# Optimization experiments

Hardware: AMD Instinct MI355X
Metric: run time of the kernel (lower is better)

Reference implementation:

```python
import jax, jax.numpy as jnp
import numpy as np


def setup_inputs() -> dict:
    key = jax.random.key(0)
    kx, kw = jax.random.split(key)
    batch, n_in, n_out = 8192, 4096, 4096
    x = jax.random.normal(kx, (batch, n_in), dtype=jnp.float32)
    stdv = 1.0 / np.sqrt(n_in)
    w = jax.random.normal(kw, (n_in, n_out), dtype=jnp.float32) * stdv
    return {"x": x, "w": w}


def reference(x, w):
    # fp16_grad forward: fp32 -> fp16 -> fp32 round trip on weights
    w16 = w.astype(jnp.float16).astype(jnp.float32)
    # binarize_weight forward: sign(clip(w, -1, 1))  (STE only affects backward)
    wb = jnp.sign(jnp.clip(w16, -1.0, 1.0))
    # dense matmul with binarized weights: [B, n_in] @ [n_in, n_out]
    return x @ wb
```

## Files before the change

### kernel.cpp

```cpp
#include <hip/hip_runtime.h>
#include <hip/hip_fp16.h>

#define MM 8192
#define NN 4096
#define KK 4096
#define BM 256
#define BN 256
#define BK 64
#define NT (KK / BK)

typedef __attribute__((ext_vector_type(8))) short bf16x8;
typedef __attribute__((ext_vector_type(4))) float floatx4;
typedef __attribute__((ext_vector_type(8))) unsigned short ushort8_t;

typedef const __attribute__((address_space(1))) unsigned int* gptr_t;
typedef __attribute__((address_space(3))) unsigned int* lptr_t;

__device__ __forceinline__ unsigned short f2bf(float f) {
    unsigned u = __builtin_bit_cast(unsigned, f);
    u += 0x7FFFu + ((u >> 16) & 1u);
    return (unsigned short)(u >> 16);
}

__device__ __forceinline__ unsigned short sign_bf16(float f) {
    float h = __half2float(__float2half(f));
    return (h > 0.f) ? 0x3F80u : ((h < 0.f) ? 0xBF80u : 0u);
}

__global__ __launch_bounds__(256) void cvt_x_kernel(const float4* __restrict__ x4,
                                                    ushort4* __restrict__ o4, int n4) {
    int i = blockIdx.x * 256 + threadIdx.x;
    if (i >= n4) return;
    float4 v = x4[i];
    ushort4 o;
    o.x = f2bf(v.x); o.y = f2bf(v.y); o.z = f2bf(v.z); o.w = f2bf(v.w);
    o4[i] = o;
}

__global__ __launch_bounds__(256) void binz_wt_kernel(const float* __restrict__ w,
                                                      unsigned short* __restrict__ wt) {
    __shared__ unsigned short tileT[64][72];
    const int n0 = blockIdx.x * 64;
    const int k0 = blockIdx.y * 64;
    const int t  = threadIdx.x;
    {
        const int c4 = t & 15;
        const int rb = t >> 4;
#pragma unroll
        for (int i = 0; i < 4; ++i) {
            int r = rb + i * 16;
            float4 v = *(const float4*)&w[(size_t)(k0 + r) * NN + n0 + c4 * 4];
            tileT[c4 * 4 + 0][r] = sign_bf16(v.x);
            tileT[c4 * 4 + 1][r] = sign_bf16(v.y);
            tileT[c4 * 4 + 2][r] = sign_bf16(v.z);
            tileT[c4 * 4 + 3][r] = sign_bf16(v.w);
        }
    }
    __syncthreads();
    {
        const int g  = t & 7;
        const int nb = t >> 3;
#pragma unroll
        for (int i = 0; i < 2; ++i) {
            int n = nb + i * 32;
            *(ushort8_t*)&wt[(size_t)(n0 + n) * KK + k0 + g * 8] =
                *(const ushort8_t*)&tileT[n][g * 8];
        }
    }
}

__global__ __launch_bounds__(512, 2) void gemm_bin_kernel(const unsigned short* __restrict__ A,
                                                          const unsigned short* __restrict__ Bt,
                                                          float* __restrict__ C) {
    __shared__ __align__(16) char lds[131072];

    const int tid    = threadIdx.x;
    const int lane   = tid & 63;
    const int wave   = tid >> 6;
    const int wave_u = __builtin_amdgcn_readfirstlane(wave);
    const int wm     = wave >> 2;
    const int wn     = wave & 3;
    const int l15    = lane & 15;
    const int kq     = lane >> 4;

    const int bid = blockIdx.x;
    const int wg  = (bid & 7) * 64 + (bid >> 3);
    const int bn0 = (wg & 15) * BN;
    const int bm0 = (wg >> 4) * BM;

    const int r0 = tid >> 3;
    const int c0 = (tid & 7) ^ (r0 & 7);
    const char* gA = (const char*)A;
    const char* gB = (const char*)Bt;
    const size_t aoff = (size_t)(bm0 + r0) * (KK * 2) + (size_t)c0 * 16;
    const size_t boff = (size_t)(bn0 + r0) * (KK * 2) + (size_t)c0 * 16;

    __attribute__((address_space(3))) char* lds3 =
        (__attribute__((address_space(3))) char*)lds;
    const int dstw = wave_u * 1024;

    const int aco0 = ((0 * 4 + kq) ^ (lane & 7)) * 16;
    const int aco1 = ((1 * 4 + kq) ^ (lane & 7)) * 16;
    const char* ldsA_l = lds + l15 * 128;
    const char* ldsB_l = lds + 65536 + ((wn & 1) * 64 + l15) * 128;

    floatx4 acc[8][4] = {};
    bf16x8 af[8][2];
    bf16x8 bfr[4][2];

    auto STAGE_A = [&](int h, int kt) {
        const int slot = (kt & 1) * 2 + h;
        const char* s0 = gA + aoff + (size_t)h * (128 * KK * 2) + (size_t)kt * (BK * 2);
        __builtin_amdgcn_global_load_lds((gptr_t)s0,
            (lptr_t)(lds3 + slot * 16384 + dstw), 16, 0, 0);
        __builtin_amdgcn_global_load_lds((gptr_t)(s0 + (size_t)64 * KK * 2),
            (lptr_t)(lds3 + slot * 16384 + 8192 + dstw), 16, 0, 0);
    };
    auto STAGE_B = [&](int h, int kt) {
        const int slot = (kt & 1) * 2 + h;
        const char* s0 = gB + boff + (size_t)h * (128 * KK * 2) + (size_t)kt * (BK * 2);
        __builtin_amdgcn_global_load_lds((gptr_t)s0,
            (lptr_t)(lds3 + 65536 + slot * 16384 + dstw), 16, 0, 0);
        __builtin_amdgcn_global_load_lds((gptr_t)(s0 + (size_t)64 * KK * 2),
            (lptr_t)(lds3 + 65536 + slot * 16384 + 8192 + dstw), 16, 0, 0);
    };
    auto LDA = [&](const char* pA, int mf) {
        af[mf][0] = *(const bf16x8*)(pA + aco0 + mf * 2048);
        af[mf][1] = *(const bf16x8*)(pA + aco1 + mf * 2048);
    };
    auto QUAD = [&](int q) {
#pragma unroll
        for (int mi = 0; mi < 2; ++mi)
#pragma unroll
            for (int nf = 0; nf < 4; ++nf)
#pragma unroll
                for (int ks = 0; ks < 2; ++ks)
                    acc[2 * q + mi][nf] = __builtin_amdgcn_mfma_f32_16x16x32_bf16(
                        af[2 * q + mi][ks], bfr[nf][ks], acc[2 * q + mi][nf], 0, 0, 0);
    };

    STAGE_B(0, 0); STAGE_B(1, 0); STAGE_A(0, 0); STAGE_A(1, 0);
    STAGE_B(0, 1); STAGE_B(1, 1); STAGE_A(0, 1);
    asm volatile("s_waitcnt vmcnt(6)" ::: "memory");
    __builtin_amdgcn_s_barrier();

    for (int t = 0; t < NT; ++t) {
        const int buf = t & 1;
        const char* pA = ldsA_l + (buf * 2 + wm) * 16384;
        const char* pB = ldsB_l + (buf * 2 + (wn >> 1)) * 16384;

#pragma unroll
        for (int nf = 0; nf < 4; ++nf) {
            bfr[nf][0] = *(const bf16x8*)(pB + aco0 + nf * 2048);
            bfr[nf][1] = *(const bf16x8*)(pB + aco1 + nf * 2048);
        }
        LDA(pA, 0); LDA(pA, 1);
        if (t + 1 < NT) STAGE_A(1, t + 1);
        __builtin_amdgcn_s_barrier();
        asm volatile("s_waitcnt lgkmcnt(0)" ::: "memory");
        __builtin_amdgcn_sched_barrier(0);
        __builtin_amdgcn_s_setprio(1);
        QUAD(0);
        __builtin_amdgcn_s_setprio(0);
        __builtin_amdgcn_s_barrier();

        LDA(pA, 2); LDA(pA, 3);
        if (t + 2 < NT) STAGE_B(0, t + 2);
        __builtin_amdgcn_s_barrier();
        asm volatile("s_waitcnt lgkmcnt(0)" ::: "memory");
        __builtin_amdgcn_sched_barrier(0);
        __builtin_amdgcn_s_setprio(1);
        QUAD(1);
        __builtin_amdgcn_s_setprio(0);
        __builtin_amdgcn_s_barrier();

        LDA(pA, 4); LDA(pA, 5); LDA(pA, 6); LDA(pA, 7);
        if (t + 2 < NT) STAGE_B(1, t + 2);
        __builtin_amdgcn_s_barrier();
        asm volatile("s_waitcnt lgkmcnt(0)" ::: "memory");
        __builtin_amdgcn_sched_barrier(0);
        __builtin_amdgcn_s_setprio(1);
        QUAD(2);
        __builtin_amdgcn_s_setprio(0);
        __builtin_amdgcn_s_barrier();

        if (t + 2 < NT) STAGE_A(0, t + 2);
        __builtin_amdgcn_s_barrier();
        __builtin_amdgcn_s_setprio(1);
        QUAD(3);
        __builtin_amdgcn_s_setprio(0);
        if (t == NT - 2) asm volatile("s_waitcnt vmcnt(0)" ::: "memory");
        else             asm volatile("s_waitcnt vmcnt(6)" ::: "memory");
        __builtin_amdgcn_s_barrier();
    }

#pragma unroll
    for (int mf = 0; mf < 8; ++mf) {
#pragma unroll
        for (int nf = 0; nf < 4; ++nf) {
            const size_t row = (size_t)(bm0 + wm * 128 + mf * 16 + kq * 4);
            const int col = bn0 + wn * 64 + nf * 16 + l15;
#pragma unroll
            for (int r = 0; r < 4; ++r)
                C[(row + r) * NN + col] = acc[mf][nf][r];
        }
    }
}

__global__ __launch_bounds__(256) void fallback_kernel(const float* __restrict__ x,
                                                       const float* __restrict__ w,
                                                       float* __restrict__ out) {
    int n = blockIdx.x * 256 + threadIdx.x;
    int m = blockIdx.y;
    float s = 0.f;
    for (int k = 0; k < KK; ++k) {
        float h = __half2float(__float2half(w[(size_t)k * NN + n]));
        float b = (h > 0.f) ? 1.f : ((h < 0.f) ? -1.f : 0.f);
        s += x[(size_t)m * KK + k] * b;
    }
    out[(size_t)m * NN + n] = s;
}

extern "C" void kernel_launch(void* const* d_in, const int* in_sizes, int n_in,
                              void* d_out, int out_size, void* d_ws, size_t ws_size,
                              hipStream_t stream) {
    const float* x = (const float*)d_in[0];
    const float* w = (const float*)d_in[1];
    if (n_in >= 2 && in_sizes[0] != MM * KK) {
        x = (const float*)d_in[1];
        w = (const float*)d_in[0];
    }
    float* out = (float*)d_out;

    const size_t xb_bytes = (size_t)MM * KK * 2;
    const size_t wt_bytes = (size_t)NN * KK * 2;

    if (ws_size >= xb_bytes + wt_bytes) {
        unsigned short* xb = (unsigned short*)d_ws;
        unsigned short* wt = (unsigned short*)((char*)d_ws + xb_bytes);

        int n4 = MM * KK / 4;
        cvt_x_kernel<<<(n4 + 255) / 256, 256, 0, stream>>>((const float4*)x, (ushort4*)xb, n4);
        binz_wt_kernel<<<dim3(NN / 64, KK / 64), 256, 0, stream>>>(w, wt);
        gemm_bin_kernel<<<dim3((NN / BN) * (MM / BM)), dim3(512), 0, stream>>>(xb, wt, out);
    } else {
        fallback_kernel<<<dim3(NN / 256, MM), 256, 0, stream>>>(x, w, out);
    }
}
```

Before: 468.2 us.

## Restructure GEMM main loop into 2x2 sub-tile quadrants with cross-tile fragment prefetch

The bf16 GEMM inner loop is rescheduled so each k-tile runs four 4x2 MFMA quadrants instead of four 2x4 row strips. The first A and B fragments of the next tile are prefetched from LDS before the last quadrant, and partial lgkmcnt waits let MFMA start while later LDS reads are still in flight. The loop is manually unrolled by two to alternate buffer pointers. The x conversion kernel also now handles eight elements per thread and writes 16-byte stores. Risks are higher register pressure and subtle ordering hazards in the hand-placed waitcnt and barrier sequence.

```diff
diff --git a/kernel.cpp b/kernel.cpp
--- a/kernel.cpp
+++ b/kernel.cpp
@@ -28,13 +28,15 @@
 }
 
 __global__ __launch_bounds__(256) void cvt_x_kernel(const float4* __restrict__ x4,
-                                                    ushort4* __restrict__ o4, int n4) {
+                                                    ushort8_t* __restrict__ o8, int n8) {
     int i = blockIdx.x * 256 + threadIdx.x;
-    if (i >= n4) return;
-    float4 v = x4[i];
-    ushort4 o;
-    o.x = f2bf(v.x); o.y = f2bf(v.y); o.z = f2bf(v.z); o.w = f2bf(v.w);
-    o4[i] = o;
+    if (i >= n8) return;
+    float4 a = x4[2 * i];
+    float4 b = x4[2 * i + 1];
+    ushort8_t o;
+    o[0] = f2bf(a.x); o[1] = f2bf(a.y); o[2] = f2bf(a.z); o[3] = f2bf(a.w);
+    o[4] = f2bf(b.x); o[5] = f2bf(b.y); o[6] = f2bf(b.z); o[7] = f2bf(b.w);
+    o8[i] = o;
 }
 
 __global__ __launch_bounds__(256) void binz_wt_kernel(const float* __restrict__ w,
@@ -103,6 +105,10 @@
     const int aco1 = ((1 * 4 + kq) ^ (lane & 7)) * 16;
     const char* ldsA_l = lds + l15 * 128;
     const char* ldsB_l = lds + 65536 + ((wn & 1) * 64 + l15) * 128;
+    const char* pA0 = ldsA_l + (0 * 2 + wm) * 16384;
+    const char* pA1 = ldsA_l + (1 * 2 + wm) * 16384;
+    const char* pB0 = ldsB_l + (0 * 2 + (wn >> 1)) * 16384;
+    const char* pB1 = ldsB_l + (1 * 2 + (wn >> 1)) * 16384;
 
     floatx4 acc[8][4] = {};
     bf16x8 af[8][2];
@@ -124,75 +130,81 @@
         __builtin_amdgcn_global_load_lds((gptr_t)(s0 + (size_t)64 * KK * 2),
             (lptr_t)(lds3 + 65536 + slot * 16384 + 8192 + dstw), 16, 0, 0);
     };
-    auto LDA = [&](const char* pA, int mf) {
-        af[mf][0] = *(const bf16x8*)(pA + aco0 + mf * 2048);
-        af[mf][1] = *(const bf16x8*)(pA + aco1 + mf * 2048);
-    };
-    auto QUAD = [&](int q) {
-#pragma unroll
-        for (int mi = 0; mi < 2; ++mi)
-#pragma unroll
-            for (int nf = 0; nf < 4; ++nf)
+    auto LDA = [&](const char* pAp, int mf) {
+        af[mf][0] = *(const bf16x8*)(pAp + aco0 + mf * 2048);
+        af[mf][1] = *(const bf16x8*)(pAp + aco1 + mf * 2048);
+    };
+    auto LDB = [&](const char* pBp, int nf) {
+        bfr[nf][0] = *(const bf16x8*)(pBp + aco0 + nf * 2048);
+        bfr[nf][1] = *(const bf16x8*)(pBp + aco1 + nf * 2048);
+    };
+    auto QUAD8 = [&](int mb, int nb) {
+#pragma unroll
+        for (int mi = 0; mi < 4; ++mi)
+#pragma unroll
+            for (int nj = 0; nj < 2; ++nj)
 #pragma unroll
                 for (int ks = 0; ks < 2; ++ks)
-                    acc[2 * q + mi][nf] = __builtin_amdgcn_mfma_f32_16x16x32_bf16(
-                        af[2 * q + mi][ks], bfr[nf][ks], acc[2 * q + mi][nf], 0, 0, 0);
-    };
+                    acc[mb + mi][nb + nj] = __builtin_amdgcn_mfma_f32_16x16x32_bf16(
+                        af[mb + mi][ks], bfr[nb + nj][ks], acc[mb + mi][nb + nj], 0, 0, 0);
+    };
+
+#define WAITL(n) do { asm volatile("s_waitcnt lgkmcnt(" #n ")" ::: "memory"); \
+                      __builtin_amdgcn_sched_barrier(0); } while (0)
 
     STAGE_B(0, 0); STAGE_B(1, 0); STAGE_A(0, 0); STAGE_A(1, 0);
     STAGE_B(0, 1); STAGE_B(1, 1); STAGE_A(0, 1);
     asm volatile("s_waitcnt vmcnt(6)" ::: "memory");
     __builtin_amdgcn_s_barrier();
-
-    for (int t = 0; t < NT; ++t) {
-        const int buf = t & 1;
-        const char* pA = ldsA_l + (buf * 2 + wm) * 16384;
-        const char* pB = ldsB_l + (buf * 2 + (wn >> 1)) * 16384;
-
-#pragma unroll
-        for (int nf = 0; nf < 4; ++nf) {
-            bfr[nf][0] = *(const bf16x8*)(pB + aco0 + nf * 2048);
-            bfr[nf][1] = *(const bf16x8*)(pB + aco1 + nf * 2048);
-        }
-        LDA(pA, 0); LDA(pA, 1);
-        if (t + 1 < NT) STAGE_A(1, t + 1);
-        __builtin_amdgcn_s_barrier();
-        asm volatile("s_waitcnt lgkmcnt(0)" ::: "memory");
-        __builtin_amdgcn_sched_barrier(0);
-        __builtin_amdgcn_s_setprio(1);
-        QUAD(0);
-        __builtin_amdgcn_s_setprio(0);
-        __builtin_amdgcn_s_barrier();
-
-        LDA(pA, 2); LDA(pA, 3);
-        if (t + 2 < NT) STAGE_B(0, t + 2);
-        __builtin_amdgcn_s_barrier();
-        asm volatile("s_waitcnt lgkmcnt(0)" ::: "memory");
-        __builtin_amdgcn_sched_barrier(0);
-        __builtin_amdgcn_s_setprio(1);
-        QUAD(1);
-        __builtin_amdgcn_s_setprio(0);
-        __builtin_amdgcn_s_barrier();
-
-        LDA(pA, 4); LDA(pA, 5); LDA(pA, 6); LDA(pA, 7);
-        if (t + 2 < NT) STAGE_B(1, t + 2);
-        __builtin_amdgcn_s_barrier();
-        asm volatile("s_waitcnt lgkmcnt(0)" ::: "memory");
-        __builtin_amdgcn_sched_barrier(0);
-        __builtin_amdgcn_s_setprio(1);
-        QUAD(2);
-        __builtin_amdgcn_s_setprio(0);
-        __builtin_amdgcn_s_barrier();
-
-        if (t + 2 < NT) STAGE_A(0, t + 2);
-        __builtin_amdgcn_s_barrier();
-        __builtin_amdgcn_s_setprio(1);
-        QUAD(3);
-        __builtin_amdgcn_s_setprio(0);
-        if (t == NT - 2) asm volatile("s_waitcnt vmcnt(0)" ::: "memory");
-        else             asm volatile("s_waitcnt vmcnt(6)" ::: "memory");
-        __builtin_amdgcn_s_barrier();
-    }
+    LDA(pA0, 0); LDA(pA0, 1); LDA(pA0, 2); LDA(pA0, 3);
+    LDB(pB0, 0); LDB(pB0, 1);
+
+#define TILE_BODY(t, pAc, pBc, pAn, pBn)                                        \
+    {                                                                           \
+                                   \
+        LDA(pAc, 4); LDA(pAc, 5); LDA(pAc, 6); LDA(pAc, 7);                     \
+        if ((t) + 1 < NT) STAGE_A(1, (t) + 1);                                  \
+        __builtin_amdgcn_s_barrier();                                           \
+        WAITL(8);                                                               \
+        __builtin_amdgcn_s_setprio(1);                                          \
+        QUAD8(0, 0);                                                            \
+        __builtin_amdgcn_s_setprio(0);                                          \
+        __builtin_amdgcn_s_barrier();                                           \
+                                  \
+        LDB(pBc, 2); LDB(pBc, 3);                                               \
+        if ((t) + 2 < NT) STAGE_B(0, (t) + 2);                                  \
+        __builtin_amdgcn_s_barrier();                                           \
+        WAITL(4);                                                               \
+        __builtin_amdgcn_s_setprio(1);                                          \
+        QUAD8(4, 0);                                                            \
+        __builtin_amdgcn_s_setprio(0);                                          \
+        __builtin_amdgcn_s_barrier();                                           \
+                        \
+        WAITL(0);                                                               \
+        __builtin_amdgcn_s_setprio(1);                                          \
+        QUAD8(0, 2);                                                            \
+        __builtin_amdgcn_s_setprio(0);                                          \
+        __builtin_amdgcn_s_barrier();                                           \
+         \
+        if ((t) + 2 < NT) { STAGE_B(1, (t) + 2); STAGE_A(0, (t) + 2); }         \
+        if ((t) == NT - 2) { asm volatile("s_waitcnt vmcnt(0)" ::: "memory"); } \
+        else               { asm volatile("s_waitcnt vmcnt(6)" ::: "memory"); } \
+        __builtin_amdgcn_s_barrier();                                           \
+        LDA(pAn, 0); LDA(pAn, 1); LDA(pAn, 2); LDA(pAn, 3);                     \
+        LDB(pBn, 0); LDB(pBn, 1);                                               \
+        WAITL(12);                                                              \
+        __builtin_amdgcn_s_setprio(1);                                          \
+        QUAD8(4, 2);                                                            \
+        __builtin_amdgcn_s_setprio(0);                                          \
+        __builtin_amdgcn_s_barrier();                                           \
+    }
+
+    for (int tb = 0; tb < NT; tb += 2) {
+        TILE_BODY(tb,     pA0, pB0, pA1, pB1);
+        TILE_BODY(tb + 1, pA1, pB1, pA0, pB0);
+    }
+#undef TILE_BODY
+#undef WAITL
 
 #pragma unroll
     for (int mf = 0; mf < 8; ++mf) {
@@ -239,8 +251,8 @@
         unsigned short* xb = (unsigned short*)d_ws;
         unsigned short* wt = (unsigned short*)((char*)d_ws + xb_bytes);
 
-        int n4 = MM * KK / 4;
-        cvt_x_kernel<<<(n4 + 255) / 256, 256, 0, stream>>>((const float4*)x, (ushort4*)xb, n4);
+        int n8 = MM * KK / 8;
+        cvt_x_kernel<<<(n8 + 255) / 256, 256, 0, stream>>>((const float4*)x, (ushort8_t*)xb, n8);
         binz_wt_kernel<<<dim3(NN / 64, KK / 64), 256, 0, stream>>>(w, wt);
         gemm_bin_kernel<<<dim3((NN / BN) * (MM / BM)), dim3(512), 0, stream>>>(xb, wt, out);
     } else {
```

Measured after the change: 468.0 us. Within noise of the previous version (-0.0%).
